# Kernel tuning notes

Hardware: AMD Instinct MI355X
Metric: run time of the kernel (lower is better)

Reference implementation:

```python
import jax, jax.numpy as jnp
import numpy as np

N_NODES = 50000
NUM_GRAPHS = 64
HID = 128
OUT = 128
NUM_LAYERS = 4


def _glorot(key, shape):
    fan_in, fan_out = shape[0], shape[1]
    lim = float(np.sqrt(6.0 / (fan_in + fan_out)))
    return jax.random.uniform(key, shape, jnp.float32, -lim, lim)


def setup_inputs() -> dict:
    key = jax.random.key(0)
    ks = jax.random.split(key, 16)
    x = jax.random.normal(ks[0], (N_NODES, HID), jnp.float32)
    edge_index = jax.random.randint(ks[1], (2, 640000), 0, N_NODES, jnp.int64)
    batch = jnp.sort(jax.random.randint(ks[2], (N_NODES,), 0, NUM_GRAPHS, jnp.int64))
    W_in = _glorot(ks[3], (HID, HID))
    b_in = jnp.zeros((HID,), jnp.float32)
    conv_W = jnp.stack([_glorot(ks[4 + i], (HID, HID)) for i in range(NUM_LAYERS)])
    conv_b = jnp.zeros((NUM_LAYERS, HID), jnp.float32)
    W_def = _glorot(ks[8], (HID, OUT)); b_def = jnp.zeros((OUT,), jnp.float32)
    W_syn = _glorot(ks[9], (HID, OUT)); b_syn = jnp.zeros((OUT,), jnp.float32)
    W_rel = _glorot(ks[10], (HID, OUT)); b_rel = jnp.zeros((OUT,), jnp.float32)
    return {"x": x, "edge_index": edge_index, "batch": batch,
            "W_in": W_in, "b_in": b_in, "conv_W": conv_W, "conv_b": conv_b,
            "W_def": W_def, "b_def": b_def, "W_syn": W_syn, "b_syn": b_syn,
            "W_rel": W_rel, "b_rel": b_rel}


def _gcn_norm(edge_index, n_nodes):
    # add self-loops, symmetric degree normalization (PyG gcn_norm defaults)
    loops = jnp.arange(n_nodes, dtype=edge_index.dtype)
    row = jnp.concatenate([edge_index[0], loops])  # source
    col = jnp.concatenate([edge_index[1], loops])  # target (aggregation index)
    deg = jax.ops.segment_sum(jnp.ones_like(col, jnp.float32), col, num_segments=n_nodes)
    dinv = jnp.where(deg > 0, jax.lax.rsqrt(jnp.maximum(deg, 1.0)), 0.0)
    norm = dinv[row] * dinv[col]  # [E+N]
    return row, col, norm


def _gcn_conv(h, row, col, norm, W, b, n_nodes):
    h = h @ W
    msg = h[row] * norm[:, None]            # gather from source, scale
    agg = jax.ops.segment_sum(msg, col, num_segments=n_nodes)  # scatter-add to target
    return agg + b


def reference(x, edge_index, batch, W_in, b_in, conv_W, conv_b,
              W_def, b_def, W_syn, b_syn, W_rel, b_rel):
    n = x.shape[0]
    row, col, norm = _gcn_norm(edge_index, n)
    h = jax.nn.relu(x @ W_in + b_in)  # dropout is identity in eval mode
    for i in range(NUM_LAYERS):
        h = jax.nn.relu(_gcn_conv(h, row, col, norm, conv_W[i], conv_b[i], n))
    # global mean pool over graphs
    sums = jax.ops.segment_sum(h, batch, num_segments=NUM_GRAPHS)
    cnts = jax.ops.segment_sum(jnp.ones((n,), jnp.float32), batch, num_segments=NUM_GRAPHS)
    pooled = sums / jnp.maximum(cnts, 1.0)[:, None]
    out_def = pooled @ W_def + b_def
    out_syn = pooled @ W_syn + b_syn
    out_rel = pooled @ W_rel + b_rel
    return (out_def, out_syn, out_rel)
```

## Files before the change

kernel.cpp:

```cpp
#include <hip/hip_runtime.h>
#include <hip/hip_bf16.h>

#define N_NODES 50000
#define NGRAPH 64
#define HID 128
#define NLAYERS 4
#define SCAN_NB ((N_NODES + 511) / 512)
#define HIST_NB 2500
#define WPREP_NB 320

typedef __attribute__((ext_vector_type(8))) __bf16 bf16x8;
typedef __attribute__((ext_vector_type(8))) unsigned short ushort8;
typedef __attribute__((ext_vector_type(4))) float f32x4;

__device__ __forceinline__ float bf2f(unsigned short u) { return __uint_as_float(((unsigned)u) << 16); }
__device__ __forceinline__ unsigned short f2bf(float f) { return __hip_bfloat16_raw(__float2bfloat16(f)).x; }
__device__ __forceinline__ float ulo(unsigned m) { return __uint_as_float(m << 16); }
__device__ __forceinline__ float uhi(unsigned m) { return __uint_as_float(m & 0xffff0000u); }

__global__ void k_init(int* __restrict__ cnt, int* __restrict__ gstart, int* __restrict__ gend) {
  int i = blockIdx.x * blockDim.x + threadIdx.x;
  if (i < N_NODES) cnt[i] = 0;
  if (i < NGRAPH) { gstart[i] = 0; gend[i] = 0; }
}

__global__ void k_hist(const int* __restrict__ col, int E, int* __restrict__ cnt,
                       const int* __restrict__ batch, int* __restrict__ gstart, int* __restrict__ gend,
                       const float* __restrict__ Win, const float* __restrict__ Wconv,
                       unsigned short* __restrict__ WtAll) {
  if (blockIdx.x < HIST_NB) {
    int e = blockIdx.x * blockDim.x + threadIdx.x;
    if (e < E) atomicAdd(&cnt[col[e]], 1);
    if (e < N_NODES) {
      int b = batch[e];
      if (e == 0 || batch[e - 1] != b) gstart[b] = e;
      if (e == N_NODES - 1 || batch[e + 1] != b) gend[b] = e + 1;
    }
  } else {
    int idx = (blockIdx.x - HIST_NB) * 256 + threadIdx.x;
    if (idx >= 5 * HID * HID) return;
    int m = idx >> 14, rem = idx & 16383;
    int k = rem >> 7, n = rem & 127;
    const float* src = (m == 0) ? Win : (Wconv + (size_t)(m - 1) * HID * HID);
    WtAll[(size_t)m * HID * HID + n * HID + k] = f2bf(src[k * HID + n]);
  }
}

__global__ __launch_bounds__(512) void k_scan1(const int* __restrict__ cnt, int* __restrict__ excl,
                                               int* __restrict__ bsum) {
  __shared__ int tmp[512];
  const int t = threadIdx.x;
  const int i = blockIdx.x * 512 + t;
  int v = (i < N_NODES) ? cnt[i] : 0;
  tmp[t] = v;
  __syncthreads();
#pragma unroll
  for (int off = 1; off < 512; off <<= 1) {
    int u = (t >= off) ? tmp[t - off] : 0;
    __syncthreads();
    tmp[t] += u;
    __syncthreads();
  }
  if (i < N_NODES) excl[i] = tmp[t] - v;
  if (t == 511) bsum[blockIdx.x] = tmp[511];
}

__global__ __launch_bounds__(128) void k_scan2(int* __restrict__ bsum, int* __restrict__ offs) {
  __shared__ int tmp[128];
  const int t = threadIdx.x;
  int v = (t < SCAN_NB) ? bsum[t] : 0;
  tmp[t] = v;
  __syncthreads();
#pragma unroll
  for (int off = 1; off < 128; off <<= 1) {
    int u = (t >= off) ? tmp[t - off] : 0;
    __syncthreads();
    tmp[t] += u;
    __syncthreads();
  }
  if (t < SCAN_NB) bsum[t] = tmp[t] - v;
  if (t == 127) offs[N_NODES] = tmp[127];
}

__global__ __launch_bounds__(512) void k_scan3(const int* __restrict__ cnt, const int* __restrict__ excl,
                                               const int* __restrict__ bsum, int* __restrict__ offs,
                                               int* __restrict__ cursor, float* __restrict__ dinv) {
  const int i = blockIdx.x * 512 + threadIdx.x;
  if (i >= N_NODES) return;
  int o = excl[i] + bsum[blockIdx.x];
  offs[i] = o;
  cursor[i] = o;
  dinv[i] = 1.0f / sqrtf((float)(cnt[i] + 1));
}

__global__ void k_fill(const int* __restrict__ row, const int* __restrict__ col, int E,
                       int* __restrict__ cursor, unsigned short* __restrict__ csr_src) {
  int e = blockIdx.x * blockDim.x + threadIdx.x;
  if (e >= E) return;
  int pos = atomicAdd(&cursor[col[e]], 1);
  csr_src[pos] = (unsigned short)row[e];
}

template <bool AF32, bool BIAS, bool RELU, bool SCALE>
__global__ __launch_bounds__(256) void k_gemm_mfma(const void* __restrict__ Av,
                                                   const unsigned short* __restrict__ Wt,
                                                   const float* __restrict__ bias,
                                                   const float* __restrict__ dinv,
                                                   unsigned short* __restrict__ Y, int M) {
  __shared__ float ys[64][132];
  const int wave = threadIdx.x >> 6;
  const int lane = threadIdx.x & 63;
  const int row16 = (blockIdx.x * 4 + wave) * 16;
  const int lr = lane & 15;
  const int lk = (lane >> 4) * 8;

  f32x4 acc[8];
#pragma unroll
  for (int i = 0; i < 8; ++i) acc[i] = (f32x4){0.f, 0.f, 0.f, 0.f};

  const int arow = min(row16 + lr, M - 1);
#pragma unroll
  for (int ks = 0; ks < 4; ++ks) {
    const int k0 = ks * 32 + lk;
    bf16x8 a;
    if (AF32) {
      const float* Af = (const float*)Av;
      float4 f0 = *(const float4*)(Af + (size_t)arow * HID + k0);
      float4 f1 = *(const float4*)(Af + (size_t)arow * HID + k0 + 4);
      ushort8 u;
      u[0] = f2bf(f0.x); u[1] = f2bf(f0.y); u[2] = f2bf(f0.z); u[3] = f2bf(f0.w);
      u[4] = f2bf(f1.x); u[5] = f2bf(f1.y); u[6] = f2bf(f1.z); u[7] = f2bf(f1.w);
      a = __builtin_bit_cast(bf16x8, u);
    } else {
      const unsigned short* Ab = (const unsigned short*)Av;
      a = *(const bf16x8*)(Ab + (size_t)arow * HID + k0);
    }
#pragma unroll
    for (int nt = 0; nt < 8; ++nt) {
      bf16x8 b = *(const bf16x8*)(Wt + (size_t)(nt * 16 + lr) * HID + k0);
      acc[nt] = __builtin_amdgcn_mfma_f32_16x16x32_bf16(a, b, acc[nt], 0, 0, 0);
    }
  }

  const int wrow = wave * 16 + (lane >> 4) * 4;
#pragma unroll
  for (int nt = 0; nt < 8; ++nt) {
    const int c = nt * 16 + lr;
#pragma unroll
    for (int r = 0; r < 4; ++r) ys[wrow + r][c] = acc[nt][r];
  }
  __syncthreads();

  const int er = threadIdx.x >> 2;
  const int q = threadIdx.x & 3;
  const int grow = blockIdx.x * 64 + er;
  if (grow < M) {
    float scale = SCALE ? dinv[grow] : 1.f;
    ushort8 pk[4];
#pragma unroll
    for (int h = 0; h < 4; ++h) {
#pragma unroll
      for (int j = 0; j < 8; ++j) {
        int c = q * 32 + h * 8 + j;
        float v = ys[er][c];
        if (BIAS) v += bias[c];
        if (RELU) v = fmaxf(v, 0.f);
        if (SCALE) v *= scale;
        pk[h][j] = f2bf(v);
      }
    }
    unsigned short* dst = Y + (size_t)grow * HID + q * 32;
    *(ushort8*)(dst)      = pk[0];
    *(ushort8*)(dst + 8)  = pk[1];
    *(ushort8*)(dst + 16) = pk[2];
    *(ushort8*)(dst + 24) = pk[3];
  }
}

__global__ __launch_bounds__(256) void k_agg(const unsigned short* __restrict__ g, const int* __restrict__ offs,
                                             const unsigned short* __restrict__ csr_src,
                                             const float* __restrict__ dinv,
                                             const float* __restrict__ bias, unsigned short* __restrict__ out) {
  const int wave = threadIdx.x >> 6;
  const int lane = threadIdx.x & 63;
  const int v = blockIdx.x * 4 + wave;
  if (v >= N_NODES) return;
  const int s = lane >> 4;
  const int c = lane & 15;

  const uint4* g4 = (const uint4*)g;

  float a0 = 0.f, a1 = 0.f, a2 = 0.f, a3 = 0.f, a4 = 0.f, a5 = 0.f, a6 = 0.f, a7 = 0.f;
  if (s == 0) {
    uint4 m = g4[(size_t)v * 16 + c];
    a0 = ulo(m.x); a1 = uhi(m.x); a2 = ulo(m.y); a3 = uhi(m.y);
    a4 = ulo(m.z); a5 = uhi(m.z); a6 = ulo(m.w); a7 = uhi(m.w);
  }

  const int lo = offs[v], hi = offs[v + 1];
  int idx = lo + s;
  for (; idx + 4 < hi; idx += 8) {
    int s0 = csr_src[idx];
    int s1 = csr_src[idx + 4];
    uint4 m0 = g4[(size_t)s0 * 16 + c];
    uint4 m1 = g4[(size_t)s1 * 16 + c];
    a0 += ulo(m0.x) + ulo(m1.x); a1 += uhi(m0.x) + uhi(m1.x);
    a2 += ulo(m0.y) + ulo(m1.y); a3 += uhi(m0.y) + uhi(m1.y);
    a4 += ulo(m0.z) + ulo(m1.z); a5 += uhi(m0.z) + uhi(m1.z);
    a6 += ulo(m0.w) + ulo(m1.w); a7 += uhi(m0.w) + uhi(m1.w);
  }
  if (idx < hi) {
    uint4 m0 = g4[(size_t)csr_src[idx] * 16 + c];
    a0 += ulo(m0.x); a1 += uhi(m0.x);
    a2 += ulo(m0.y); a3 += uhi(m0.y);
    a4 += ulo(m0.z); a5 += uhi(m0.z);
    a6 += ulo(m0.w); a7 += uhi(m0.w);
  }

  a0 += __shfl_xor(a0, 16, 64); a0 += __shfl_xor(a0, 32, 64);
  a1 += __shfl_xor(a1, 16, 64); a1 += __shfl_xor(a1, 32, 64);
  a2 += __shfl_xor(a2, 16, 64); a2 += __shfl_xor(a2, 32, 64);
  a3 += __shfl_xor(a3, 16, 64); a3 += __shfl_xor(a3, 32, 64);
  a4 += __shfl_xor(a4, 16, 64); a4 += __shfl_xor(a4, 32, 64);
  a5 += __shfl_xor(a5, 16, 64); a5 += __shfl_xor(a5, 32, 64);
  a6 += __shfl_xor(a6, 16, 64); a6 += __shfl_xor(a6, 32, 64);
  a7 += __shfl_xor(a7, 16, 64); a7 += __shfl_xor(a7, 32, 64);

  if (s == 0) {
    const float d = dinv[v];
    float4 b0 = ((const float4*)bias)[c * 2];
    float4 b1 = ((const float4*)bias)[c * 2 + 1];
    float o0 = fmaxf(d * a0 + b0.x, 0.f), o1 = fmaxf(d * a1 + b0.y, 0.f);
    float o2 = fmaxf(d * a2 + b0.z, 0.f), o3 = fmaxf(d * a3 + b0.w, 0.f);
    float o4 = fmaxf(d * a4 + b1.x, 0.f), o5 = fmaxf(d * a5 + b1.y, 0.f);
    float o6 = fmaxf(d * a6 + b1.z, 0.f), o7 = fmaxf(d * a7 + b1.w, 0.f);
    uint4 pk;
    pk.x = (unsigned)f2bf(o0) | ((unsigned)f2bf(o1) << 16);
    pk.y = (unsigned)f2bf(o2) | ((unsigned)f2bf(o3) << 16);
    pk.z = (unsigned)f2bf(o4) | ((unsigned)f2bf(o5) << 16);
    pk.w = (unsigned)f2bf(o6) | ((unsigned)f2bf(o7) << 16);
    ((uint4*)out)[(size_t)v * 16 + c] = pk;
  }
}

__global__ __launch_bounds__(1024) void k_poolheads(const unsigned short* __restrict__ h,
                                                    const int* __restrict__ gstart, const int* __restrict__ gend,
                                                    const float* __restrict__ W0, const float* __restrict__ b0,
                                                    const float* __restrict__ W1, const float* __restrict__ b1,
                                                    const float* __restrict__ W2, const float* __restrict__ b2,
                                                    float* __restrict__ out) {
  __shared__ float red[1024];
  __shared__ float pm[HID];
  const int g = blockIdx.x;
  const int tid = threadIdx.x;
  const int j = tid & 127;
  const int r0 = tid >> 7;
  const int lo = gstart[g], hi = gend[g];
  float acc = 0.f;
  for (int v = lo + r0; v < hi; v += 8) acc += bf2f(h[(size_t)v * HID + j]);
  red[tid] = acc;
  __syncthreads();
  if (r0 < 4) red[tid] += red[tid + 512];
  __syncthreads();
  if (r0 < 2) red[tid] += red[tid + 256];
  __syncthreads();
  if (r0 < 1) {
    float s = red[tid] + red[tid + 128];
    pm[j] = s / fmaxf((float)(hi - lo), 1.f);
  }
  __syncthreads();
  if (tid < 384) {
    const int t = tid >> 7;
    const int cc = tid & 127;
    const float* W = (t == 0) ? W0 : ((t == 1) ? W1 : W2);
    const float* b = (t == 0) ? b0 : ((t == 1) ? b1 : b2);
    float a2 = 0.f;
#pragma unroll 8
    for (int k = 0; k < HID; ++k) a2 += pm[k] * W[k * HID + cc];
    out[((size_t)t * NGRAPH + g) * HID + cc] = a2 + b[cc];
  }
}

extern "C" void kernel_launch(void* const* d_in, const int* in_sizes, int n_in,
                              void* d_out, int out_size, void* d_ws, size_t ws_size,
                              hipStream_t stream) {
  const float* x     = (const float*)d_in[0];
  const int*   ei    = (const int*)d_in[1];
  const int*   batch = (const int*)d_in[2];
  const float* W_in  = (const float*)d_in[3];
  const float* b_in  = (const float*)d_in[4];
  const float* convW = (const float*)d_in[5];
  const float* convb = (const float*)d_in[6];
  const float* W_def = (const float*)d_in[7];
  const float* b_def = (const float*)d_in[8];
  const float* W_syn = (const float*)d_in[9];
  const float* b_syn = (const float*)d_in[10];
  const float* W_rel = (const float*)d_in[11];
  const float* b_rel = (const float*)d_in[12];

  const int E = in_sizes[1] / 2;
  const int* row = ei;
  const int* col = ei + E;

  char* base = (char*)d_ws;
  size_t off = 0;
  auto alloc = [&](size_t bytes) -> void* {
    void* p = base + off;
    off += (bytes + 255) & ~size_t(255);
    return p;
  };
  int*   cnt     = (int*)  alloc((size_t)N_NODES * 4);
  float* dinv    = (float*)alloc((size_t)N_NODES * 4);
  int*   offs    = (int*)  alloc((size_t)(N_NODES + 1) * 4);
  int*   cursor  = (int*)  alloc((size_t)N_NODES * 4);
  int*   excl    = (int*)  alloc((size_t)N_NODES * 4);
  int*   bsum    = (int*)  alloc((size_t)SCAN_NB * 4);
  unsigned short* csr_src = (unsigned short*)alloc((size_t)E * 2);
  unsigned short* hA = (unsigned short*)alloc((size_t)N_NODES * HID * 2);
  unsigned short* hB = (unsigned short*)alloc((size_t)N_NODES * HID * 2);
  unsigned short* WtAll = (unsigned short*)alloc((size_t)5 * HID * HID * 2);
  int*   gstart  = (int*)  alloc((size_t)NGRAPH * 4);
  int*   gend    = (int*)  alloc((size_t)NGRAPH * 4);

  k_init<<<(N_NODES + 255) / 256, 256, 0, stream>>>(cnt, gstart, gend);
  k_hist<<<HIST_NB + WPREP_NB, 256, 0, stream>>>(col, E, cnt, batch, gstart, gend, W_in, convW, WtAll);
  k_scan1<<<SCAN_NB, 512, 0, stream>>>(cnt, excl, bsum);
  k_scan2<<<1, 128, 0, stream>>>(bsum, offs);
  k_scan3<<<SCAN_NB, 512, 0, stream>>>(cnt, excl, bsum, offs, cursor, dinv);
  k_fill<<<(E + 255) / 256, 256, 0, stream>>>(row, col, E, cursor, csr_src);

  const int gemm_grid = (N_NODES + 63) / 64;
  k_gemm_mfma<true, true, true, false><<<gemm_grid, 256, 0, stream>>>(x, WtAll, b_in, nullptr, hA, N_NODES);

  for (int i = 0; i < NLAYERS; ++i) {
    k_gemm_mfma<false, false, false, true><<<gemm_grid, 256, 0, stream>>>(
        hA, WtAll + (size_t)(i + 1) * HID * HID, nullptr, dinv, hB, N_NODES);
    k_agg<<<(N_NODES + 3) / 4, 256, 0, stream>>>(hB, offs, csr_src, dinv, convb + (size_t)i * HID, hA);
  }

  k_poolheads<<<NGRAPH, 1024, 0, stream>>>(hA, gstart, gend, W_def, b_def, W_syn, b_syn, W_rel, b_rel,
                                           (float*)d_out);
}
```

Baseline: 346.8 us.

## Partition histogram and CSR fill atomics by destination-node range per block

The degree histogram and the CSR fill now assign each block one of 8 destination-node partitions plus an edge chunk. Each block scans its chunk and only does atomics on targets inside its partition, so the atomics from a block hit a smaller address range, likely aimed at L2 locality on an XCD-partitioned GPU. The cost is that every edge's col value is read 8 times, and row is read for the matching entries. Batch-boundary detection is moved into its own block range.

```diff
diff --git a/kernel.cpp b/kernel.cpp
--- a/kernel.cpp
+++ b/kernel.cpp
@@ -6,7 +6,10 @@
 #define HID 128
 #define NLAYERS 4
 #define SCAN_NB ((N_NODES + 511) / 512)
-#define HIST_NB 2500
+#define NPART 8
+#define COLS_PER_PART (N_NODES / NPART)
+#define HCHUNK 80
+#define BOUNDS_NB ((N_NODES + 255) / 256)
 #define WPREP_NB 320
 
 typedef __attribute__((ext_vector_type(8))) __bf16 bf16x8;
@@ -24,20 +27,30 @@
   if (i < NGRAPH) { gstart[i] = 0; gend[i] = 0; }
 }
 
-__global__ void k_hist(const int* __restrict__ col, int E, int* __restrict__ cnt,
-                       const int* __restrict__ batch, int* __restrict__ gstart, int* __restrict__ gend,
-                       const float* __restrict__ Win, const float* __restrict__ Wconv,
-                       unsigned short* __restrict__ WtAll) {
-  if (blockIdx.x < HIST_NB) {
-    int e = blockIdx.x * blockDim.x + threadIdx.x;
-    if (e < E) atomicAdd(&cnt[col[e]], 1);
-    if (e < N_NODES) {
-      int b = batch[e];
-      if (e == 0 || batch[e - 1] != b) gstart[b] = e;
-      if (e == N_NODES - 1 || batch[e + 1] != b) gend[b] = e + 1;
+__global__ void k_pre(const int* __restrict__ col, int E, int* __restrict__ cnt,
+                      const int* __restrict__ batch, int* __restrict__ gstart, int* __restrict__ gend,
+                      const float* __restrict__ Win, const float* __restrict__ Wconv,
+                      unsigned short* __restrict__ WtAll) {
+  const int bid = blockIdx.x;
+  if (bid < NPART * HCHUNK) {
+    const int p = bid % NPART;
+    const int chunk = bid / NPART;
+    const int clo = p * COLS_PER_PART, chi = clo + COLS_PER_PART;
+    const int chunkE = (E + HCHUNK - 1) / HCHUNK;
+    const int elo = chunk * chunkE, ehi = min(elo + chunkE, E);
+    for (int e = elo + threadIdx.x; e < ehi; e += 256) {
+      int c = col[e];
+      if (c >= clo && c < chi) atomicAdd(&cnt[c], 1);
+    }
+  } else if (bid < NPART * HCHUNK + BOUNDS_NB) {
+    int i = (bid - NPART * HCHUNK) * 256 + threadIdx.x;
+    if (i < N_NODES) {
+      int b = batch[i];
+      if (i == 0 || batch[i - 1] != b) gstart[b] = i;
+      if (i == N_NODES - 1 || batch[i + 1] != b) gend[b] = i + 1;
     }
   } else {
-    int idx = (blockIdx.x - HIST_NB) * 256 + threadIdx.x;
+    int idx = (bid - NPART * HCHUNK - BOUNDS_NB) * 256 + threadIdx.x;
     if (idx >= 5 * HID * HID) return;
     int m = idx >> 14, rem = idx & 16383;
     int k = rem >> 7, n = rem & 127;
@@ -95,10 +108,18 @@
 
 __global__ void k_fill(const int* __restrict__ row, const int* __restrict__ col, int E,
                        int* __restrict__ cursor, unsigned short* __restrict__ csr_src) {
-  int e = blockIdx.x * blockDim.x + threadIdx.x;
-  if (e >= E) return;
-  int pos = atomicAdd(&cursor[col[e]], 1);
-  csr_src[pos] = (unsigned short)row[e];
+  const int p = blockIdx.x % NPART;
+  const int chunk = blockIdx.x / NPART;
+  const int clo = p * COLS_PER_PART, chi = clo + COLS_PER_PART;
+  const int chunkE = (E + HCHUNK - 1) / HCHUNK;
+  const int elo = chunk * chunkE, ehi = min(elo + chunkE, E);
+  for (int e = elo + threadIdx.x; e < ehi; e += 256) {
+    int c = col[e];
+    if (c >= clo && c < chi) {
+      int pos = atomicAdd(&cursor[c], 1);
+      csr_src[pos] = (unsigned short)row[e];
+    }
+  }
 }
 
 template <bool AF32, bool BIAS, bool RELU, bool SCALE>
@@ -323,11 +344,12 @@
   int*   gend    = (int*)  alloc((size_t)NGRAPH * 4);
 
   k_init<<<(N_NODES + 255) / 256, 256, 0, stream>>>(cnt, gstart, gend);
-  k_hist<<<HIST_NB + WPREP_NB, 256, 0, stream>>>(col, E, cnt, batch, gstart, gend, W_in, convW, WtAll);
+  k_pre<<<NPART * HCHUNK + BOUNDS_NB + WPREP_NB, 256, 0, stream>>>(
+      col, E, cnt, batch, gstart, gend, W_in, convW, WtAll);
   k_scan1<<<SCAN_NB, 512, 0, stream>>>(cnt, excl, bsum);
   k_scan2<<<1, 128, 0, stream>>>(bsum, offs);
   k_scan3<<<SCAN_NB, 512, 0, stream>>>(cnt, excl, bsum, offs, cursor, dinv);
-  k_fill<<<(E + 255) / 256, 256, 0, stream>>>(row, col, E, cursor, csr_src);
+  k_fill<<<NPART * HCHUNK, 256, 0, stream>>>(row, col, E, cursor, csr_src);
 
   const int gemm_grid = (N_NODES + 63) / 64;
   k_gemm_mfma<true, true, true, false><<<gemm_grid, 256, 0, stream>>>(x, WtAll, b_in, nullptr, hA, N_NODES);
```

After: 350.8 us. About the same (+1.2%).

## Fuse GCN aggregation with next layer's GEMM via shared-memory tile

Applied to the files above, without the earlier changes.

Adds a kernel that aggregates neighbour features for a 64-node tile into LDS (with bias, ReLU, bf16), then multiplies by the next layer's weights with MFMA and writes the dinv-scaled result. This replaces three separate agg and GEMM launches, removing the intermediate h write and reread. The price is lower parallelism in the aggregation: 8 waves per 64 nodes instead of 4 nodes per block, so gather latency hiding and load balance may suffer. A third ping-pong buffer is added.

```diff
diff --git a/kernel.cpp b/kernel.cpp
--- a/kernel.cpp
+++ b/kernel.cpp
@@ -240,6 +240,110 @@
     pk.z = (unsigned)f2bf(o4) | ((unsigned)f2bf(o5) << 16);
     pk.w = (unsigned)f2bf(o6) | ((unsigned)f2bf(o7) << 16);
     ((uint4*)out)[(size_t)v * 16 + c] = pk;
+  }
+}
+
+__global__ __launch_bounds__(512) void k_agggemm(const unsigned short* __restrict__ g,
+                                                 const int* __restrict__ offs,
+                                                 const unsigned short* __restrict__ csr_src,
+                                                 const float* __restrict__ dinv,
+                                                 const float* __restrict__ bias,
+                                                 const unsigned short* __restrict__ Wt,
+                                                 unsigned short* __restrict__ gout) {
+  __shared__ unsigned short hs[64][136];
+  const int wid = threadIdx.x >> 6;
+  const int lane = threadIdx.x & 63;
+  const int s = lane >> 4;
+  const int c = lane & 15;
+  const int tile = blockIdx.x * 64;
+  const uint4* g4 = (const uint4*)g;
+
+  for (int it = 0; it < 8; ++it) {
+    const int vloc = wid * 8 + it;
+    const int v = tile + vloc;
+    if (v >= N_NODES) break;
+
+    float a0 = 0.f, a1 = 0.f, a2 = 0.f, a3 = 0.f, a4 = 0.f, a5 = 0.f, a6 = 0.f, a7 = 0.f;
+    if (s == 0) {
+      uint4 m = g4[(size_t)v * 16 + c];
+      a0 = ulo(m.x); a1 = uhi(m.x); a2 = ulo(m.y); a3 = uhi(m.y);
+      a4 = ulo(m.z); a5 = uhi(m.z); a6 = ulo(m.w); a7 = uhi(m.w);
+    }
+    const int lo = offs[v], hi = offs[v + 1];
+    int idx = lo + s;
+    for (; idx + 4 < hi; idx += 8) {
+      int s0 = csr_src[idx];
+      int s1 = csr_src[idx + 4];
+      uint4 m0 = g4[(size_t)s0 * 16 + c];
+      uint4 m1 = g4[(size_t)s1 * 16 + c];
+      a0 += ulo(m0.x) + ulo(m1.x); a1 += uhi(m0.x) + uhi(m1.x);
+      a2 += ulo(m0.y) + ulo(m1.y); a3 += uhi(m0.y) + uhi(m1.y);
+      a4 += ulo(m0.z) + ulo(m1.z); a5 += uhi(m0.z) + uhi(m1.z);
+      a6 += ulo(m0.w) + ulo(m1.w); a7 += uhi(m0.w) + uhi(m1.w);
+    }
+    if (idx < hi) {
+      uint4 m0 = g4[(size_t)csr_src[idx] * 16 + c];
+      a0 += ulo(m0.x); a1 += uhi(m0.x);
+      a2 += ulo(m0.y); a3 += uhi(m0.y);
+      a4 += ulo(m0.z); a5 += uhi(m0.z);
+      a6 += ulo(m0.w); a7 += uhi(m0.w);
+    }
+    a0 += __shfl_xor(a0, 16, 64); a0 += __shfl_xor(a0, 32, 64);
+    a1 += __shfl_xor(a1, 16, 64); a1 += __shfl_xor(a1, 32, 64);
+    a2 += __shfl_xor(a2, 16, 64); a2 += __shfl_xor(a2, 32, 64);
+    a3 += __shfl_xor(a3, 16, 64); a3 += __shfl_xor(a3, 32, 64);
+    a4 += __shfl_xor(a4, 16, 64); a4 += __shfl_xor(a4, 32, 64);
+    a5 += __shfl_xor(a5, 16, 64); a5 += __shfl_xor(a5, 32, 64);
+    a6 += __shfl_xor(a6, 16, 64); a6 += __shfl_xor(a6, 32, 64);
+    a7 += __shfl_xor(a7, 16, 64); a7 += __shfl_xor(a7, 32, 64);
+
+    if (s == 0) {
+      const float d = dinv[v];
+      float4 b0 = ((const float4*)bias)[c * 2];
+      float4 b1 = ((const float4*)bias)[c * 2 + 1];
+      float o0 = fmaxf(d * a0 + b0.x, 0.f), o1 = fmaxf(d * a1 + b0.y, 0.f);
+      float o2 = fmaxf(d * a2 + b0.z, 0.f), o3 = fmaxf(d * a3 + b0.w, 0.f);
+      float o4 = fmaxf(d * a4 + b1.x, 0.f), o5 = fmaxf(d * a5 + b1.y, 0.f);
+      float o6 = fmaxf(d * a6 + b1.z, 0.f), o7 = fmaxf(d * a7 + b1.w, 0.f);
+      uint4 pk;
+      pk.x = (unsigned)f2bf(o0) | ((unsigned)f2bf(o1) << 16);
+      pk.y = (unsigned)f2bf(o2) | ((unsigned)f2bf(o3) << 16);
+      pk.z = (unsigned)f2bf(o4) | ((unsigned)f2bf(o5) << 16);
+      pk.w = (unsigned)f2bf(o6) | ((unsigned)f2bf(o7) << 16);
+      *(uint4*)&hs[vloc][c * 8] = pk;
+    }
+  }
+  __syncthreads();
+
+  const int mt = wid & 3;
+  const int nb = (wid >> 2) * 4;
+  const int lr = lane & 15;
+  const int lk = (lane >> 4) * 8;
+
+  f32x4 acc[4];
+#pragma unroll
+  for (int j = 0; j < 4; ++j) acc[j] = (f32x4){0.f, 0.f, 0.f, 0.f};
+
+#pragma unroll
+  for (int ks = 0; ks < 4; ++ks) {
+    const int k0 = ks * 32 + lk;
+    bf16x8 a = *(const bf16x8*)&hs[mt * 16 + lr][k0];
+#pragma unroll
+    for (int j = 0; j < 4; ++j) {
+      bf16x8 b = *(const bf16x8*)(Wt + (size_t)((nb + j) * 16 + lr) * HID + k0);
+      acc[j] = __builtin_amdgcn_mfma_f32_16x16x32_bf16(a, b, acc[j], 0, 0, 0);
+    }
+  }
+
+  const int drow = tile + mt * 16 + (lane >> 4) * 4;
+#pragma unroll
+  for (int j = 0; j < 4; ++j) {
+    const int gcol = (nb + j) * 16 + lr;
+#pragma unroll
+    for (int r = 0; r < 4; ++r) {
+      const int rr = drow + r;
+      if (rr < N_NODES) gout[(size_t)rr * HID + gcol] = f2bf(acc[j][r] * dinv[rr]);
+    }
   }
 }
 
@@ -318,6 +422,7 @@
   unsigned short* csr_src = (unsigned short*)alloc((size_t)E * 2);
   unsigned short* hA = (unsigned short*)alloc((size_t)N_NODES * HID * 2);
   unsigned short* hB = (unsigned short*)alloc((size_t)N_NODES * HID * 2);
+  unsigned short* hC = (unsigned short*)alloc((size_t)N_NODES * HID * 2);
   unsigned short* WtAll = (unsigned short*)alloc((size_t)5 * HID * HID * 2);
   int*   gstart  = (int*)  alloc((size_t)NGRAPH * 4);
   int*   gend    = (int*)  alloc((size_t)NGRAPH * 4);
@@ -331,12 +436,20 @@
 
   const int gemm_grid = (N_NODES + 63) / 64;
   k_gemm_mfma<true, true, true, false><<<gemm_grid, 256, 0, stream>>>(x, WtAll, b_in, nullptr, hA, N_NODES);
-
-  for (int i = 0; i < NLAYERS; ++i) {
-    k_gemm_mfma<false, false, false, true><<<gemm_grid, 256, 0, stream>>>(
-        hA, WtAll + (size_t)(i + 1) * HID * HID, nullptr, dinv, hB, N_NODES);
-    k_agg<<<(N_NODES + 3) / 4, 256, 0, stream>>>(hB, offs, csr_src, dinv, convb + (size_t)i * HID, hA);
-  }
+  k_gemm_mfma<false, false, false, true><<<gemm_grid, 256, 0, stream>>>(
+      hA, WtAll + (size_t)1 * HID * HID, nullptr, dinv, hB, N_NODES);
+
+  unsigned short* gin = hB;
+  unsigned short* gout = hC;
+  for (int i = 0; i < 3; ++i) {
+    k_agggemm<<<gemm_grid, 512, 0, stream>>>(gin, offs, csr_src, dinv,
+                                             convb + (size_t)i * HID,
+                                             WtAll + (size_t)(i + 2) * HID * HID, gout);
+    unsigned short* t = gin; gin = gout; gout = t;
+  }
+
+  k_agg<<<(N_NODES + 3) / 4, 256, 0, stream>>>(gin, offs, csr_src, dinv,
+                                               convb + (size_t)3 * HID, hA);
 
   k_poolheads<<<NGRAPH, 1024, 0, stream>>>(hA, gstart, gend, W_def, b_def, W_syn, b_syn, W_rel, b_rel,
                                            (float*)d_out);
```

Result: faster. 326.1 us (-6.0%).
